# Optimization experiments

Hardware: AMD Instinct MI355X
Metric: run time of the kernel (lower is better)

Reference implementation:

```python
import jax, jax.numpy as jnp
import numpy as np

B, S, HID = 2, 2048, 1024
H, D = 16, HID // 16  # heads, head_dim
ROPE_BASE = 10000.0


def setup_inputs() -> dict:
    key = jax.random.key(0)
    k1, k2, k3, k4 = jax.random.split(key, 4)
    scale = 1.0 / np.sqrt(HID)
    return {
        "hidden_states": jax.random.normal(k1, (B, S, HID), dtype=jnp.float32),
        "attention_mask": jnp.zeros((B, 1, 1, S), dtype=jnp.float32),
        "Wq": jax.random.normal(k2, (HID, HID), dtype=jnp.float32) * scale,
        "Wk": jax.random.normal(k3, (HID, HID), dtype=jnp.float32) * scale,
        "Wv": jax.random.normal(k4, (HID, HID), dtype=jnp.float32) * scale,
    }


def _rope_cos_sin(seq_len, dim, dtype):
    inv_freq = 1.0 / (ROPE_BASE ** (jnp.arange(0, dim, 2, dtype=jnp.float32) / dim))
    freqs = jnp.arange(seq_len, dtype=jnp.float32)[:, None] * inv_freq[None, :]  # (S, D/2)
    emb = jnp.concatenate([freqs, freqs], axis=-1)  # (S, D)
    return jnp.cos(emb).astype(dtype), jnp.sin(emb).astype(dtype)


def _rotate_half(x):
    x1, x2 = jnp.split(x, 2, axis=-1)
    return jnp.concatenate([-x2, x1], axis=-1)


def reference(hidden_states, attention_mask, Wq, Wk, Wv):
    b, s, _ = hidden_states.shape
    # QKV projections (no bias), split into heads: (b, H, s, D)
    def proj(W):
        return jnp.einsum('bse,de->bsd', hidden_states, W).reshape(b, s, H, D).transpose(0, 2, 1, 3)
    q, k, v = proj(Wq), proj(Wk), proj(Wv)
    # Rotary embedding on q, k over sequence positions
    cos, sin = _rope_cos_sin(s, D, hidden_states.dtype)  # (s, D)
    cos = cos[None, None]  # (1,1,s,D)
    sin = sin[None, None]
    q = q * cos + _rotate_half(q) * sin
    k = k * cos + _rotate_half(k) * sin
    # Scaled dot-product attention with additive mask
    scores = jnp.einsum('bhqd,bhkd->bhqk', q, k) / jnp.sqrt(jnp.asarray(D, hidden_states.dtype))
    scores = scores + attention_mask
    probs = jax.nn.softmax(scores, axis=-1)  # dropout p=0 (eval) -> identity
    ctx = jnp.einsum('bhqk,bhkd->bhqd', probs, v)
    return ctx.transpose(0, 2, 1, 3).reshape(b, s, H * D)
```

## Files before the change

kernel.cpp:

```cpp
#include <hip/hip_runtime.h>
#include <stdint.h>

typedef unsigned short u16;
typedef short bf16x8 __attribute__((ext_vector_type(8)));
typedef float f32x4 __attribute__((ext_vector_type(4)));

#define S_ 2048
#define HID_ 1024
#define H_ 16
#define D_ 64

#define LOG2E 1.4426950408889634f
#define SCALE_LOG2 0.18033688011112042f
#define MAXC_LOG2 11.541560327111707f

__device__ __forceinline__ u16 f2bf(float f) {
  uint32_t x = __builtin_bit_cast(uint32_t, f);
  uint32_t r = (x + 0x7fffu + ((x >> 16) & 1u)) >> 16;
  return (u16)r;
}
__device__ __forceinline__ uint32_t packbf2(float a, float b) {
  return (uint32_t)f2bf(a) | ((uint32_t)f2bf(b) << 16);
}

__device__ __forceinline__ void gl2lds16(const void* g, void* l) {
  __builtin_amdgcn_global_load_lds(
      (const __attribute__((address_space(1))) unsigned int*)g,
      (__attribute__((address_space(3))) unsigned int*)l, 16, 0, 0);
}

#define NX_ (1 << 20)
#define NW_ (1 << 18)
__global__ void prep_kernel(const float* __restrict__ X, const float* __restrict__ Wq,
                            const float* __restrict__ Wk, const float* __restrict__ Wv,
                            u16* __restrict__ Xb, u16* __restrict__ Wqb,
                            u16* __restrict__ Wkb, u16* __restrict__ Wvb,
                            float* __restrict__ cos_t, float* __restrict__ sin_t) {
  int i = blockIdx.x * 256 + threadIdx.x;
  if (i < NX_ + 3 * NW_) {
    const float* src;
    u16* dst;
    int off;
    if (i < NX_) {
      src = X; dst = Xb; off = i;
    } else if (i < NX_ + NW_) {
      src = Wq; dst = Wqb; off = i - NX_;
    } else if (i < NX_ + 2 * NW_) {
      src = Wk; dst = Wkb; off = i - NX_ - NW_;
    } else {
      src = Wv; dst = Wvb; off = i - NX_ - 2 * NW_;
    }
    float4 v = ((const float4*)src)[off];
    uint2 packed;
    packed.x = packbf2(v.x, v.y);
    packed.y = packbf2(v.z, v.w);
    ((uint2*)dst)[off] = packed;
  } else {
    int t = i - (NX_ + 3 * NW_);
    int s = t >> 5, j = t & 31;
    float invf = powf(10000.0f, -(float)j * (1.0f / 32.0f));
    float ang = (float)s * invf;
    cos_t[t] = cosf(ang);
    sin_t[t] = sinf(ang);
  }
}

__global__ __launch_bounds__(256) void qkv_gemm_kernel(
    const u16* __restrict__ X, const u16* __restrict__ Wq, const u16* __restrict__ Wk,
    const u16* __restrict__ Wv, const float* __restrict__ cos_t,
    const float* __restrict__ sin_t, u16* __restrict__ Q, u16* __restrict__ K,
    u16* __restrict__ Vt) {
  __shared__ char smem[65536];
  int tid = threadIdx.x;
  int lane = tid & 63, wave = tid >> 6;
  int wm = wave >> 1, wn = wave & 1;
  int quad = lane >> 4, l16 = lane & 15;
  int which = blockIdx.x >> 3;
  int nbase = (blockIdx.x & 7) * 128;
  int mbase = blockIdx.y * 128;
  const u16* W = (which == 0) ? Wq : (which == 1) ? Wk : Wv;

  {
#pragma unroll
    for (int it = 0; it < 4; ++it) {
      int i = it * 256 + tid;
      int r = i >> 3, gs = i & 7, gsrc = gs ^ (r & 7);
      gl2lds16(X + (size_t)(mbase + r) * HID_ + gsrc * 8, smem + i * 16);
      gl2lds16(W + (size_t)(nbase + r) * HID_ + gsrc * 8, smem + 32768 + i * 16);
    }
  }

  f32x4 acc[4][4] = {};

  for (int kk = 0; kk < 16; ++kk) {
    char* As = smem + (kk & 1) * 16384;
    char* Bs = smem + 32768 + (kk & 1) * 16384;
    __syncthreads();

    if (kk < 15) {
      int k0n = (kk + 1) * 64;
      char* An = smem + ((kk + 1) & 1) * 16384;
      char* Bn = smem + 32768 + ((kk + 1) & 1) * 16384;
#pragma unroll
      for (int it = 0; it < 4; ++it) {
        int i = it * 256 + tid;
        int r = i >> 3, gs = i & 7, gsrc = gs ^ (r & 7);
        gl2lds16(X + (size_t)(mbase + r) * HID_ + k0n + gsrc * 8, An + i * 16);
        gl2lds16(W + (size_t)(nbase + r) * HID_ + k0n + gsrc * 8, Bn + i * 16);
      }
    }

#pragma unroll
    for (int kh = 0; kh < 2; ++kh) {
      bf16x8 afrag[4], bfrag[4];
#pragma unroll
      for (int i4 = 0; i4 < 4; ++i4) {
        int r = wm * 64 + i4 * 16 + l16;
        int L = r * 8 + ((kh * 4 + quad) ^ (r & 7));
        afrag[i4] = *(const bf16x8*)(As + L * 16);
      }
#pragma unroll
      for (int j4 = 0; j4 < 4; ++j4) {
        int r = wn * 64 + j4 * 16 + l16;
        int L = r * 8 + ((kh * 4 + quad) ^ (r & 7));
        bfrag[j4] = *(const bf16x8*)(Bs + L * 16);
      }
      if (which == 2) {
#pragma unroll
        for (int i4 = 0; i4 < 4; ++i4)
#pragma unroll
          for (int j4 = 0; j4 < 4; ++j4)
            acc[i4][j4] = __builtin_amdgcn_mfma_f32_16x16x32_bf16(afrag[i4], bfrag[j4],
                                                                  acc[i4][j4], 0, 0, 0);
      } else {
#pragma unroll
        for (int i4 = 0; i4 < 4; ++i4)
#pragma unroll
          for (int j4 = 0; j4 < 4; ++j4)
            acc[i4][j4] = __builtin_amdgcn_mfma_f32_16x16x32_bf16(bfrag[j4], afrag[i4],
                                                                  acc[i4][j4], 0, 0, 0);
      }
    }
  }

  if (which == 2) {
#pragma unroll
    for (int i4 = 0; i4 < 4; ++i4)
#pragma unroll
      for (int j4 = 0; j4 < 4; ++j4) {
        int m = mbase + wm * 64 + i4 * 16 + quad * 4;
        int n = nbase + wn * 64 + j4 * 16 + l16;
        int b = m >> 11, s0 = m & 2047;
        int h = n >> 6, d = n & 63;
        uint2 pk;
        pk.x = packbf2(acc[i4][j4][0], acc[i4][j4][1]);
        pk.y = packbf2(acc[i4][j4][2], acc[i4][j4][3]);
        *(uint2*)(Vt + (((size_t)(b * H_ + h)) * D_ + d) * S_ + s0) = pk;
      }
  } else {
    u16* dst = (which == 0) ? Q : K;
#pragma unroll
    for (int i4 = 0; i4 < 4; ++i4)
#pragma unroll
      for (int j4 = 0; j4 < 2; ++j4) {
        int m = mbase + wm * 64 + i4 * 16 + l16;
        int n1 = nbase + wn * 64 + j4 * 16 + quad * 4;
        int b = m >> 11, s = m & 2047;
        int h = n1 >> 6, d1 = n1 & 63;
        float4 c4 = *(const float4*)(cos_t + s * 32 + d1);
        float4 s4 = *(const float4*)(sin_t + s * 32 + d1);
        float y1[4], y2[4];
#pragma unroll
        for (int r = 0; r < 4; ++r) {
          float cr = ((const float*)&c4)[r], sr = ((const float*)&s4)[r];
          float x1 = acc[i4][j4][r], x2 = acc[i4][j4 + 2][r];
          y1[r] = x1 * cr - x2 * sr;
          y2[r] = x2 * cr + x1 * sr;
        }
        size_t base = ((size_t)(b * H_ + h) * S_ + s) * D_;
        uint2 p1, p2;
        p1.x = packbf2(y1[0], y1[1]);
        p1.y = packbf2(y1[2], y1[3]);
        p2.x = packbf2(y2[0], y2[1]);
        p2.y = packbf2(y2[2], y2[3]);
        *(uint2*)(dst + base + d1) = p1;
        *(uint2*)(dst + base + d1 + 32) = p2;
      }
  }
}

__global__ __launch_bounds__(256) void flash_kernel(
    const u16* __restrict__ Q, const u16* __restrict__ K, const u16* __restrict__ Vt,
    const float* __restrict__ mask, float* __restrict__ out) {
  __shared__ char smem[49152];
  int tid = threadIdx.x, lane = tid & 63, wave = tid >> 6;
  int quad = lane >> 4, l16 = lane & 15;
  int bh = blockIdx.y, b = bh >> 4, h = bh & 15;
  int qbase = blockIdx.x * 128;
  int qw = qbase + wave * 32;
  char* Pw = smem + 32768 + wave * 4096;
  const float* mrow = mask + b * S_;
  const u16* Kbase = K + (size_t)bh * S_ * D_;
  const u16* Vbase = Vt + (size_t)bh * D_ * S_;

  bf16x8 qfrag[2][2];
#pragma unroll
  for (int g = 0; g < 2; ++g) {
    const u16* qp = Q + ((size_t)bh * S_ + qw + g * 16 + l16) * D_ + quad * 8;
    qfrag[g][0] = *(const bf16x8*)qp;
    qfrag[g][1] = *(const bf16x8*)(qp + 32);
  }
  f32x4 o0[4] = {}, o1[4] = {};
  float l0 = 0.f, l1 = 0.f;

#pragma unroll
  for (int it = 0; it < 2; ++it) {
    int i = it * 256 + tid;
    int r = i >> 3, gs = i & 7, gsrc = gs ^ (r & 7);
    gl2lds16(Kbase + (size_t)r * D_ + gsrc * 8, smem + i * 16);
    gl2lds16(Vbase + (size_t)r * S_ + gsrc * 8, smem + 8192 + i * 16);
  }

  for (int kt = 0; kt < 32; ++kt) {
    int kbase = kt * 64;
    char* Ks = smem + (kt & 1) * 16384;
    char* Vs = Ks + 8192;
    __syncthreads();

    if (kt < 31) {
      char* Kn = smem + ((kt + 1) & 1) * 16384;
      char* Vn = Kn + 8192;
      int nb = kbase + 64;
#pragma unroll
      for (int it = 0; it < 2; ++it) {
        int i = it * 256 + tid;
        int r = i >> 3, gs = i & 7, gsrc = gs ^ (r & 7);
        gl2lds16(Kbase + (size_t)(nb + r) * D_ + gsrc * 8, Kn + i * 16);
        gl2lds16(Vbase + (size_t)r * S_ + nb + gsrc * 8, Vn + i * 16);
      }
    }

    float4 mv4[4];
#pragma unroll
    for (int jt = 0; jt < 4; ++jt)
      mv4[jt] = *(const float4*)(mrow + kbase + jt * 16 + quad * 4);

    f32x4 s0[4] = {}, s1[4] = {};
#pragma unroll
    for (int jt = 0; jt < 4; ++jt) {
      int r = jt * 16 + l16;
#pragma unroll
      for (int kh = 0; kh < 2; ++kh) {
        int L = r * 8 + ((kh * 4 + quad) ^ (r & 7));
        bf16x8 kf = *(const bf16x8*)(Ks + L * 16);
        s0[jt] = __builtin_amdgcn_mfma_f32_16x16x32_bf16(kf, qfrag[0][kh], s0[jt], 0, 0, 0);
        s1[jt] = __builtin_amdgcn_mfma_f32_16x16x32_bf16(kf, qfrag[1][kh], s1[jt], 0, 0, 0);
      }
    }

#pragma unroll
    for (int jt = 0; jt < 4; ++jt) {
      float mvs[4];
#pragma unroll
      for (int r = 0; r < 4; ++r)
        mvs[r] = fmaf(((const float*)&mv4[jt])[r], LOG2E, -MAXC_LOG2);
      uint32_t bt0[4], bt1[4];
#pragma unroll
      for (int r = 0; r < 4; ++r) {
        float p0 = __builtin_amdgcn_exp2f(fmaf(s0[jt][r], SCALE_LOG2, mvs[r]));
        float p1 = __builtin_amdgcn_exp2f(fmaf(s1[jt][r], SCALE_LOG2, mvs[r]));
        bt0[r] = __builtin_bit_cast(uint32_t, p0) & 0xffff0000u;
        bt1[r] = __builtin_bit_cast(uint32_t, p1) & 0xffff0000u;
        l0 += __builtin_bit_cast(float, bt0[r]);
        l1 += __builtin_bit_cast(float, bt1[r]);
      }
      int chunk = (jt * 4 + quad) ^ l16;
      uint2 pk0, pk1;
      pk0.x = (bt0[0] >> 16) | bt0[1];
      pk0.y = (bt0[2] >> 16) | bt0[3];
      pk1.x = (bt1[0] >> 16) | bt1[1];
      pk1.y = (bt1[2] >> 16) | bt1[3];
      *(uint2*)(Pw + l16 * 128 + chunk * 8) = pk0;
      *(uint2*)(Pw + 2048 + l16 * 128 + chunk * 8) = pk1;
    }

    bf16x8 p0[2], p1[2];
#pragma unroll
    for (int kh = 0; kh < 2; ++kh) {
      int c0 = kh * 8 + quad * 2;
      union { uint2 u[2]; bf16x8 v; } cv0, cv1;
      cv0.u[0] = *(const uint2*)(Pw + l16 * 128 + ((c0) ^ l16) * 8);
      cv0.u[1] = *(const uint2*)(Pw + l16 * 128 + ((c0 + 1) ^ l16) * 8);
      cv1.u[0] = *(const uint2*)(Pw + 2048 + l16 * 128 + ((c0) ^ l16) * 8);
      cv1.u[1] = *(const uint2*)(Pw + 2048 + l16 * 128 + ((c0 + 1) ^ l16) * 8);
      p0[kh] = cv0.v;
      p1[kh] = cv1.v;
    }

#pragma unroll
    for (int jd = 0; jd < 4; ++jd) {
      int r = jd * 16 + l16;
#pragma unroll
      for (int kh = 0; kh < 2; ++kh) {
        int L = r * 8 + ((kh * 4 + quad) ^ (r & 7));
        bf16x8 vf = *(const bf16x8*)(Vs + L * 16);
        o0[jd] = __builtin_amdgcn_mfma_f32_16x16x32_bf16(p0[kh], vf, o0[jd], 0, 0, 0);
        o1[jd] = __builtin_amdgcn_mfma_f32_16x16x32_bf16(p1[kh], vf, o1[jd], 0, 0, 0);
      }
    }
  }

#pragma unroll
  for (int g = 0; g < 2; ++g) {
    float lsum = g ? l1 : l0;
    lsum += __shfl_xor(lsum, 16, 64);
    lsum += __shfl_xor(lsum, 32, 64);
    float inv_l[4];
#pragma unroll
    for (int r = 0; r < 4; ++r) inv_l[r] = 1.0f / __shfl(lsum, quad * 4 + r, 64);
    f32x4* o = g ? o1 : o0;
#pragma unroll
    for (int jd = 0; jd < 4; ++jd) {
#pragma unroll
      for (int r = 0; r < 4; ++r) {
        int q = qw + g * 16 + quad * 4 + r;
        int d = jd * 16 + l16;
        out[(((size_t)b * S_ + q) * H_ + h) * D_ + d] = o[jd][r] * inv_l[r];
      }
    }
  }
}

extern "C" void kernel_launch(void* const* d_in, const int* in_sizes, int n_in,
                              void* d_out, int out_size, void* d_ws, size_t ws_size,
                              hipStream_t stream) {
  const float* hid = (const float*)d_in[0];
  const float* mask = (const float*)d_in[1];
  const float* Wq = (const float*)d_in[2];
  const float* Wk = (const float*)d_in[3];
  const float* Wv = (const float*)d_in[4];
  float* out = (float*)d_out;
  char* ws = (char*)d_ws;

  u16* Xbf = (u16*)ws;
  u16* Wqb = (u16*)(ws + (8u << 20));
  u16* Wkb = (u16*)(ws + (10u << 20));
  u16* Wvb = (u16*)(ws + (12u << 20));
  u16* Qb = (u16*)(ws + (14u << 20));
  u16* Kb = (u16*)(ws + (22u << 20));
  u16* Vtb = (u16*)(ws + (30u << 20));
  float* cos_t = (float*)(ws + (38u << 20));
  float* sin_t = (float*)(ws + (38u << 20) + (256u << 10));

  prep_kernel<<<7424, 256, 0, stream>>>(hid, Wq, Wk, Wv, Xbf, Wqb, Wkb, Wvb, cos_t, sin_t);
  qkv_gemm_kernel<<<dim3(24, 32), 256, 0, stream>>>(Xbf, Wqb, Wkb, Wvb, cos_t, sin_t,
                                                    Qb, Kb, Vtb);
  flash_kernel<<<dim3(16, 32), 256, 0, stream>>>(Qb, Kb, Vtb, mask, out);
}
```

Measured before the change: 179.4 us.

## Load W fragments from global, compute row sums via MFMA, premultiply mask

```diff
diff --git a/kernel.cpp b/kernel.cpp
--- a/kernel.cpp
+++ b/kernel.cpp
@@ -22,6 +22,10 @@
 __device__ __forceinline__ uint32_t packbf2(float a, float b) {
   return (uint32_t)f2bf(a) | ((uint32_t)f2bf(b) << 16);
 }
+__device__ __forceinline__ uint32_t permpack(float a, float b) {
+  return __builtin_amdgcn_perm(__builtin_bit_cast(uint32_t, b),
+                               __builtin_bit_cast(uint32_t, a), 0x07060302u);
+}
 
 __device__ __forceinline__ void gl2lds16(const void* g, void* l) {
   __builtin_amdgcn_global_load_lds(
@@ -31,11 +35,13 @@
 
 #define NX_ (1 << 20)
 #define NW_ (1 << 18)
+#define NROPE_ 65536
 __global__ void prep_kernel(const float* __restrict__ X, const float* __restrict__ Wq,
                             const float* __restrict__ Wk, const float* __restrict__ Wv,
-                            u16* __restrict__ Xb, u16* __restrict__ Wqb,
-                            u16* __restrict__ Wkb, u16* __restrict__ Wvb,
-                            float* __restrict__ cos_t, float* __restrict__ sin_t) {
+                            const float* __restrict__ mask, u16* __restrict__ Xb,
+                            u16* __restrict__ Wqb, u16* __restrict__ Wkb,
+                            u16* __restrict__ Wvb, float* __restrict__ cos_t,
+                            float* __restrict__ sin_t, float* __restrict__ mask2) {
   int i = blockIdx.x * 256 + threadIdx.x;
   if (i < NX_ + 3 * NW_) {
     const float* src;
@@ -55,13 +61,16 @@
     packed.x = packbf2(v.x, v.y);
     packed.y = packbf2(v.z, v.w);
     ((uint2*)dst)[off] = packed;
-  } else {
+  } else if (i < NX_ + 3 * NW_ + NROPE_) {
     int t = i - (NX_ + 3 * NW_);
     int s = t >> 5, j = t & 31;
     float invf = powf(10000.0f, -(float)j * (1.0f / 32.0f));
     float ang = (float)s * invf;
     cos_t[t] = cosf(ang);
     sin_t[t] = sinf(ang);
+  } else {
+    int t = i - (NX_ + 3 * NW_ + NROPE_);
+    mask2[t] = fmaf(mask[t], LOG2E, -MAXC_LOG2);
   }
 }
 
@@ -70,7 +79,7 @@
     const u16* __restrict__ Wv, const float* __restrict__ cos_t,
     const float* __restrict__ sin_t, u16* __restrict__ Q, u16* __restrict__ K,
     u16* __restrict__ Vt) {
-  __shared__ char smem[65536];
+  __shared__ char smem[32768];
   int tid = threadIdx.x;
   int lane = tid & 63, wave = tid >> 6;
   int wm = wave >> 1, wn = wave & 1;
@@ -80,64 +89,64 @@
   int mbase = blockIdx.y * 128;
   const u16* W = (which == 0) ? Wq : (which == 1) ? Wk : Wv;
 
-  {
-#pragma unroll
-    for (int it = 0; it < 4; ++it) {
-      int i = it * 256 + tid;
-      int r = i >> 3, gs = i & 7, gsrc = gs ^ (r & 7);
-      gl2lds16(X + (size_t)(mbase + r) * HID_ + gsrc * 8, smem + i * 16);
-      gl2lds16(W + (size_t)(nbase + r) * HID_ + gsrc * 8, smem + 32768 + i * 16);
-    }
+  const u16* wrow[4];
+#pragma unroll
+  for (int j4 = 0; j4 < 4; ++j4)
+    wrow[j4] = W + (size_t)(nbase + wn * 64 + j4 * 16 + l16) * HID_ + quad * 8;
+
+#pragma unroll
+  for (int it = 0; it < 4; ++it) {
+    int i = it * 256 + tid;
+    int r = i >> 3, gs = i & 7, gsrc = gs ^ (r & 7);
+    gl2lds16(X + (size_t)(mbase + r) * HID_ + gsrc * 8, smem + i * 16);
   }
 
   f32x4 acc[4][4] = {};
 
   for (int kk = 0; kk < 16; ++kk) {
     char* As = smem + (kk & 1) * 16384;
-    char* Bs = smem + 32768 + (kk & 1) * 16384;
     __syncthreads();
+
+    bf16x8 bfrag[2][4];
+#pragma unroll
+    for (int kh = 0; kh < 2; ++kh)
+#pragma unroll
+      for (int j4 = 0; j4 < 4; ++j4)
+        bfrag[kh][j4] = *(const bf16x8*)(wrow[j4] + kk * 64 + kh * 32);
 
     if (kk < 15) {
       int k0n = (kk + 1) * 64;
       char* An = smem + ((kk + 1) & 1) * 16384;
-      char* Bn = smem + 32768 + ((kk + 1) & 1) * 16384;
 #pragma unroll
       for (int it = 0; it < 4; ++it) {
         int i = it * 256 + tid;
         int r = i >> 3, gs = i & 7, gsrc = gs ^ (r & 7);
         gl2lds16(X + (size_t)(mbase + r) * HID_ + k0n + gsrc * 8, An + i * 16);
-        gl2lds16(W + (size_t)(nbase + r) * HID_ + k0n + gsrc * 8, Bn + i * 16);
       }
     }
 
 #pragma unroll
     for (int kh = 0; kh < 2; ++kh) {
-      bf16x8 afrag[4], bfrag[4];
+      bf16x8 afrag[4];
 #pragma unroll
       for (int i4 = 0; i4 < 4; ++i4) {
         int r = wm * 64 + i4 * 16 + l16;
         int L = r * 8 + ((kh * 4 + quad) ^ (r & 7));
         afrag[i4] = *(const bf16x8*)(As + L * 16);
       }
-#pragma unroll
-      for (int j4 = 0; j4 < 4; ++j4) {
-        int r = wn * 64 + j4 * 16 + l16;
-        int L = r * 8 + ((kh * 4 + quad) ^ (r & 7));
-        bfrag[j4] = *(const bf16x8*)(Bs + L * 16);
-      }
       if (which == 2) {
 #pragma unroll
         for (int i4 = 0; i4 < 4; ++i4)
 #pragma unroll
           for (int j4 = 0; j4 < 4; ++j4)
-            acc[i4][j4] = __builtin_amdgcn_mfma_f32_16x16x32_bf16(afrag[i4], bfrag[j4],
+            acc[i4][j4] = __builtin_amdgcn_mfma_f32_16x16x32_bf16(afrag[i4], bfrag[kh][j4],
                                                                   acc[i4][j4], 0, 0, 0);
       } else {
 #pragma unroll
         for (int i4 = 0; i4 < 4; ++i4)
 #pragma unroll
           for (int j4 = 0; j4 < 4; ++j4)
-            acc[i4][j4] = __builtin_amdgcn_mfma_f32_16x16x32_bf16(bfrag[j4], afrag[i4],
+            acc[i4][j4] = __builtin_amdgcn_mfma_f32_16x16x32_bf16(bfrag[kh][j4], afrag[i4],
                                                                   acc[i4][j4], 0, 0, 0);
       }
     }
@@ -191,15 +200,16 @@
 
 __global__ __launch_bounds__(256) void flash_kernel(
     const u16* __restrict__ Q, const u16* __restrict__ K, const u16* __restrict__ Vt,
-    const float* __restrict__ mask, float* __restrict__ out) {
+    const float* __restrict__ mask2, float* __restrict__ out) {
   __shared__ char smem[49152];
-  int tid = threadIdx.x, lane = tid & 63, wave = tid >> 6;
+  int tid = threadIdx.x, wave = tid >> 6;
+  int lane = tid & 63;
   int quad = lane >> 4, l16 = lane & 15;
   int bh = blockIdx.y, b = bh >> 4, h = bh & 15;
   int qbase = blockIdx.x * 128;
   int qw = qbase + wave * 32;
   char* Pw = smem + 32768 + wave * 4096;
-  const float* mrow = mask + b * S_;
+  const float* m2row = mask2 + b * S_;
   const u16* Kbase = K + (size_t)bh * S_ * D_;
   const u16* Vbase = Vt + (size_t)bh * D_ * S_;
 
@@ -210,8 +220,12 @@
     qfrag[g][0] = *(const bf16x8*)qp;
     qfrag[g][1] = *(const bf16x8*)(qp + 32);
   }
+  bf16x8 ones;
+#pragma unroll
+  for (int j = 0; j < 8; ++j) ones[j] = (short)0x3f80;
+
   f32x4 o0[4] = {}, o1[4] = {};
-  float l0 = 0.f, l1 = 0.f;
+  f32x4 lacc0 = {}, lacc1 = {};
 
 #pragma unroll
   for (int it = 0; it < 2; ++it) {
@@ -243,7 +257,7 @@
     float4 mv4[4];
 #pragma unroll
     for (int jt = 0; jt < 4; ++jt)
-      mv4[jt] = *(const float4*)(mrow + kbase + jt * 16 + quad * 4);
+      mv4[jt] = *(const float4*)(m2row + kbase + jt * 16 + quad * 4);
 
     f32x4 s0[4] = {}, s1[4] = {};
 #pragma unroll
@@ -260,26 +274,19 @@
 
 #pragma unroll
     for (int jt = 0; jt < 4; ++jt) {
-      float mvs[4];
-#pragma unroll
-      for (int r = 0; r < 4; ++r)
-        mvs[r] = fmaf(((const float*)&mv4[jt])[r], LOG2E, -MAXC_LOG2);
-      uint32_t bt0[4], bt1[4];
+      float p0f[4], p1f[4];
 #pragma unroll
       for (int r = 0; r < 4; ++r) {
-        float p0 = __builtin_amdgcn_exp2f(fmaf(s0[jt][r], SCALE_LOG2, mvs[r]));
-        float p1 = __builtin_amdgcn_exp2f(fmaf(s1[jt][r], SCALE_LOG2, mvs[r]));
-        bt0[r] = __builtin_bit_cast(uint32_t, p0) & 0xffff0000u;
-        bt1[r] = __builtin_bit_cast(uint32_t, p1) & 0xffff0000u;
-        l0 += __builtin_bit_cast(float, bt0[r]);
-        l1 += __builtin_bit_cast(float, bt1[r]);
-      }
+        float mv = ((const float*)&mv4[jt])[r];
+        p0f[r] = __builtin_amdgcn_exp2f(fmaf(s0[jt][r], SCALE_LOG2, mv));
+        p1f[r] = __builtin_amdgcn_exp2f(fmaf(s1[jt][r], SCALE_LOG2, mv));
+      }
+      uint2 pk0, pk1;
+      pk0.x = permpack(p0f[0], p0f[1]);
+      pk0.y = permpack(p0f[2], p0f[3]);
+      pk1.x = permpack(p1f[0], p1f[1]);
+      pk1.y = permpack(p1f[2], p1f[3]);
       int chunk = (jt * 4 + quad) ^ l16;
-      uint2 pk0, pk1;
-      pk0.x = (bt0[0] >> 16) | bt0[1];
-      pk0.y = (bt0[2] >> 16) | bt0[3];
-      pk1.x = (bt1[0] >> 16) | bt1[1];
-      pk1.y = (bt1[2] >> 16) | bt1[3];
       *(uint2*)(Pw + l16 * 128 + chunk * 8) = pk0;
       *(uint2*)(Pw + 2048 + l16 * 128 + chunk * 8) = pk1;
     }
@@ -297,6 +304,11 @@
       p1[kh] = cv1.v;
     }
 
+    lacc0 = __builtin_amdgcn_mfma_f32_16x16x32_bf16(p0[0], ones, lacc0, 0, 0, 0);
+    lacc0 = __builtin_amdgcn_mfma_f32_16x16x32_bf16(p0[1], ones, lacc0, 0, 0, 0);
+    lacc1 = __builtin_amdgcn_mfma_f32_16x16x32_bf16(p1[0], ones, lacc1, 0, 0, 0);
+    lacc1 = __builtin_amdgcn_mfma_f32_16x16x32_bf16(p1[1], ones, lacc1, 0, 0, 0);
+
 #pragma unroll
     for (int jd = 0; jd < 4; ++jd) {
       int r = jd * 16 + l16;
@@ -310,23 +322,21 @@
     }
   }
 
-#pragma unroll
-  for (int g = 0; g < 2; ++g) {
-    float lsum = g ? l1 : l0;
-    lsum += __shfl_xor(lsum, 16, 64);
-    lsum += __shfl_xor(lsum, 32, 64);
-    float inv_l[4];
-#pragma unroll
-    for (int r = 0; r < 4; ++r) inv_l[r] = 1.0f / __shfl(lsum, quad * 4 + r, 64);
-    f32x4* o = g ? o1 : o0;
-#pragma unroll
-    for (int jd = 0; jd < 4; ++jd) {
-#pragma unroll
-      for (int r = 0; r < 4; ++r) {
-        int q = qw + g * 16 + quad * 4 + r;
-        int d = jd * 16 + l16;
-        out[(((size_t)b * S_ + q) * H_ + h) * D_ + d] = o[jd][r] * inv_l[r];
-      }
+  float inv0[4], inv1[4];
+#pragma unroll
+  for (int r = 0; r < 4; ++r) {
+    inv0[r] = 1.0f / lacc0[r];
+    inv1[r] = 1.0f / lacc1[r];
+  }
+#pragma unroll
+  for (int jd = 0; jd < 4; ++jd) {
+#pragma unroll
+    for (int r = 0; r < 4; ++r) {
+      int d = jd * 16 + l16;
+      int q0 = qw + quad * 4 + r;
+      out[(((size_t)b * S_ + q0) * H_ + h) * D_ + d] = o0[jd][r] * inv0[r];
+      int q1 = qw + 16 + quad * 4 + r;
+      out[(((size_t)b * S_ + q1) * H_ + h) * D_ + d] = o1[jd][r] * inv1[r];
     }
   }
 }
@@ -351,9 +361,11 @@
   u16* Vtb = (u16*)(ws + (30u << 20));
   float* cos_t = (float*)(ws + (38u << 20));
   float* sin_t = (float*)(ws + (38u << 20) + (256u << 10));
-
-  prep_kernel<<<7424, 256, 0, stream>>>(hid, Wq, Wk, Wv, Xbf, Wqb, Wkb, Wvb, cos_t, sin_t);
+  float* mask2 = (float*)(ws + (38u << 20) + (512u << 10));
+
+  prep_kernel<<<7440, 256, 0, stream>>>(hid, Wq, Wk, Wv, mask, Xbf, Wqb, Wkb, Wvb,
+                                        cos_t, sin_t, mask2);
   qkv_gemm_kernel<<<dim3(24, 32), 256, 0, stream>>>(Xbf, Wqb, Wkb, Wvb, cos_t, sin_t,
                                                     Qb, Kb, Vtb);
-  flash_kernel<<<dim3(16, 32), 256, 0, stream>>>(Qb, Kb, Vtb, mask, out);
-}
+  flash_kernel<<<dim3(16, 32), 256, 0, stream>>>(Qb, Kb, Vtb, mask2, out);
+}
```

Result: slower. 218.5 us (+21.8%).
